# Optimization experiments

Hardware: AMD Instinct MI355X
Metric: run time of the kernel (lower is better)

Reference implementation:

```python
import jax, jax.numpy as jnp
import numpy as np

BETA = 0.9
THRESHOLD = 1.0


def setup_inputs() -> dict:
    key = jax.random.key(0)
    k1, k2 = jax.random.split(key)
    T, N_IN, N_OUT = 1024, 4096, 4096
    x = jax.random.normal(k1, (T, N_IN), dtype=jnp.float32)
    # fc1 weight initialized uniform[0,1), shape [out, in] like nn.Linear
    W = jax.random.uniform(k2, (N_OUT, N_IN), dtype=jnp.float32)
    return {"x": x, "W": W}


def reference(x, W):
    # Precompute the batched linear projection over all timesteps: [T, N_OUT]
    cur = jnp.einsum('ti,oi->to', x, W)
    mem0 = jnp.zeros((W.shape[0],), dtype=x.dtype)

    def step(mem, c):
        # snntorch Leaky, reset_mechanism='subtract':
        # reset is computed from the PREVIOUS membrane potential (detached)
        reset = (mem > THRESHOLD).astype(mem.dtype)
        mem_new = BETA * mem + c - reset * THRESHOLD
        spk = (mem_new > THRESHOLD).astype(mem.dtype)
        return mem_new, (spk, mem_new)

    _, (spk_rec, mem_rec) = jax.lax.scan(step, mem0, cur)
    return spk_rec, mem_rec
```

## Files before the change

kernel.cpp:

```cpp
#include <hip/hip_runtime.h>
#include <hip/hip_bf16.h>
#include <stdint.h>


typedef __attribute__((ext_vector_type(8))) short bf16x8;
typedef __attribute__((ext_vector_type(4))) float floatx4;

#define T_STEPS 1024
#define N_IN    4096
#define N_OUT   4096

#define PH_T 128
#define NPH  (T_STEPS / PH_T)
#define NB_N 16
#define TP   132

#define TN ((size_t)T_STEPS * N_OUT)

__device__ __forceinline__ unsigned short f2bf_rne(float f) {
    unsigned int u = __builtin_bit_cast(unsigned int, f);
    unsigned int r = 0x7FFFu + ((u >> 16) & 1u);
    return (unsigned short)((u + r) >> 16);
}

__global__ __launch_bounds__(256) void cvt2_kernel(const float4* __restrict__ inX,
                                                   ushort4* __restrict__ outX, int n4x,
                                                   const float4* __restrict__ inW,
                                                   ushort4* __restrict__ outW, int n4w) {
    int i = blockIdx.x * blockDim.x + threadIdx.x;
    const float4* in;
    ushort4* out;
    int k;
    if (i < n4x) { in = inX; out = outX; k = i; }
    else         { in = inW; out = outW; k = i - n4x; if (k >= n4w) return; }
    float4 v = in[k];
    ushort4 o;
    o.x = f2bf_rne(v.x);
    o.y = f2bf_rne(v.y);
    o.z = f2bf_rne(v.z);
    o.w = f2bf_rne(v.w);
    out[k] = o;
}

__device__ __forceinline__ void gload16(const void* g, void* l) {
    __builtin_amdgcn_global_load_lds((const __attribute__((address_space(1))) void*)g,
                                     (__attribute__((address_space(3))) void*)l,
                                     16, 0, 0);
}

#define SB0()  __builtin_amdgcn_sched_barrier(0)
#define BARR() __builtin_amdgcn_s_barrier()

__global__ __launch_bounds__(512, 2) void gemm8(const short* __restrict__ A,
                                                const short* __restrict__ B,
                                                unsigned short* __restrict__ Pb,
                                                int kLen) {
    __shared__ short lds[65536];

    const int tid  = threadIdx.x;
    const int lane = tid & 63;
    const int wv   = tid >> 6;
    const int wm   = (wv >> 2) * 128;
    const int wn   = (wv & 3) * 64;

    const int bid  = blockIdx.x;
    const int z    = bid >> 6;
    const int tile = bid & 63;
    const long bm  = (long)(tile >> 4) * 256;
    const long bn  = (long)(tile & 15) * 256;
    const int kBeg = z * kLen;
    unsigned short* __restrict__ Pz = Pb + (size_t)z * TN;
    const int NT    = kLen / 64;
    const int NITER = NT / 2;

    const int srow = lane >> 3;
    const int scol = ((lane & 7) ^ srow) << 3;
    const short* aSrc = A + (bm + wv * 8 + srow) * (long)N_IN + kBeg + scol;
    const short* bSrc = B + (bn + wv * 8 + srow) * (long)N_IN + kBeg + scol;
    const int ldA = wv * 512;
    const int ldB = 32768 + wv * 512;

    const int fm    = lane & 15;
    const int fko   = (lane >> 4) * 8;
    const int cbase = fko ^ ((fm & 7) << 3);

    floatx4 acc[8][4] = {};
    bf16x8 af[4][2];
    bf16x8 bq[2][2][2];

    auto loadA = [&](int b, int qm) {
#pragma unroll
        for (int mi = 0; mi < 4; ++mi)
#pragma unroll
            for (int ks = 0; ks < 2; ++ks)
                af[mi][ks] = *(const bf16x8*)(
                    lds + b * 16384 + (wm + qm * 64 + mi * 16 + fm) * 64 +
                    (cbase ^ (ks << 5)));
    };
    auto loadB = [&](int b, int qn) {
#pragma unroll
        for (int nj = 0; nj < 2; ++nj)
#pragma unroll
            for (int ks = 0; ks < 2; ++ks)
                bq[qn][nj][ks] = *(const bf16x8*)(
                    lds + 32768 + b * 16384 + (wn + qn * 32 + nj * 16 + fm) * 64 +
                    (cbase ^ (ks << 5)));
    };
    auto mfma16 = [&](int qm, int qn) {
        __builtin_amdgcn_s_setprio(1);
#pragma unroll
        for (int ks = 0; ks < 2; ++ks)
#pragma unroll
            for (int mi = 0; mi < 4; ++mi)
#pragma unroll
                for (int nj = 0; nj < 2; ++nj)
                    acc[qm * 4 + mi][qn * 2 + nj] =
                        __builtin_amdgcn_mfma_f32_16x16x32_bf16(
                            af[mi][ks], bq[qn][nj][ks],
                            acc[qm * 4 + mi][qn * 2 + nj], 0, 0, 0);
        __builtin_amdgcn_s_setprio(0);
    };
    auto stageA = [&](int b, int h, int t) {
        const short* s = aSrc + (size_t)(h * 128) * N_IN + t * 64;
        gload16(s,                    lds + b * 16384 + h * 8192 + ldA);
        gload16(s + (size_t)64 * N_IN, lds + b * 16384 + h * 8192 + 4096 + ldA);
    };
    auto stageB = [&](int b, int h, int t) {
        const short* s = bSrc + (size_t)(h * 128) * N_IN + t * 64;
        gload16(s,                    lds + b * 16384 + h * 8192 + ldB);
        gload16(s + (size_t)64 * N_IN, lds + b * 16384 + h * 8192 + 4096 + ldB);
    };
    const int cn = lane & 15;
    const int cm = (lane >> 4) * 4;
    auto storeQuad = [&](int qm, int qn) {
#pragma unroll
        for (int mi = 0; mi < 4; ++mi)
#pragma unroll
            for (int nj = 0; nj < 2; ++nj) {
                const floatx4 a = acc[qm * 4 + mi][qn * 2 + nj];
                unsigned int lo = (unsigned int)f2bf_rne(a[0]) |
                                  ((unsigned int)f2bf_rne(a[1]) << 16);
                unsigned int hi = (unsigned int)f2bf_rne(a[2]) |
                                  ((unsigned int)f2bf_rne(a[3]) << 16);
                uint2 v; v.x = lo; v.y = hi;
                size_t nIdx = (size_t)(bn + wn + qn * 32 + nj * 16 + cn);
                *(uint2*)(Pz + nIdx * T_STEPS +
                          (size_t)(bm + wm + qm * 64 + mi * 16 + cm)) = v;
            }
    };

    stageA(0, 0, 0); stageA(0, 1, 0);
    stageB(0, 0, 0); stageB(0, 1, 0);
    stageB(1, 0, 1); stageB(1, 1, 1);
    asm volatile("s_waitcnt vmcnt(4)" ::: "memory");
    SB0();
    BARR();

    for (int i = 0; i < NITER - 1; ++i) {
        const int t1 = 2 * i + 1;
        const int t2 = 2 * i + 2;
        const int t3 = 2 * i + 3;

        loadA(0, 0); loadB(0, 0);
        stageA(1, 0, t1);
        asm volatile("s_waitcnt lgkmcnt(8)" ::: "memory");
        SB0(); BARR();
        asm volatile("s_waitcnt lgkmcnt(0)" ::: "memory"); SB0();
        mfma16(0, 0);
        SB0(); BARR();

        loadB(0, 1);
        stageA(1, 1, t1);
        SB0(); BARR();
        asm volatile("s_waitcnt lgkmcnt(0)" ::: "memory"); SB0();
        mfma16(0, 1);
        SB0(); BARR();

        loadA(0, 1);
        stageB(0, 0, t2);
        SB0(); BARR();
        asm volatile("s_waitcnt lgkmcnt(0)" ::: "memory"); SB0();
        mfma16(1, 0);
        SB0(); BARR();

        stageB(0, 1, t2);
        SB0(); BARR();
        mfma16(1, 1);
        asm volatile("s_waitcnt vmcnt(4)" ::: "memory");
        SB0(); BARR();

        loadA(1, 0); loadB(1, 0);
        stageA(0, 0, t2);
        asm volatile("s_waitcnt lgkmcnt(8)" ::: "memory");
        SB0(); BARR();
        asm volatile("s_waitcnt lgkmcnt(0)" ::: "memory"); SB0();
        mfma16(0, 0);
        SB0(); BARR();

        loadB(1, 1);
        stageA(0, 1, t2);
        SB0(); BARR();
        asm volatile("s_waitcnt lgkmcnt(0)" ::: "memory"); SB0();
        mfma16(0, 1);
        SB0(); BARR();

        loadA(1, 1);
        stageB(1, 0, t3);
        SB0(); BARR();
        asm volatile("s_waitcnt lgkmcnt(0)" ::: "memory"); SB0();
        mfma16(1, 0);
        SB0(); BARR();

        stageB(1, 1, t3);
        SB0(); BARR();
        mfma16(1, 1);
        asm volatile("s_waitcnt vmcnt(4)" ::: "memory");
        SB0(); BARR();
    }

    {
        const int t1 = 2 * (NITER - 1) + 1;

        loadA(0, 0); loadB(0, 0);
        stageA(1, 0, t1);
        asm volatile("s_waitcnt lgkmcnt(8)" ::: "memory");
        SB0(); BARR();
        asm volatile("s_waitcnt lgkmcnt(0)" ::: "memory"); SB0();
        mfma16(0, 0);
        SB0(); BARR();

        loadB(0, 1);
        stageA(1, 1, t1);
        SB0(); BARR();
        asm volatile("s_waitcnt lgkmcnt(0)" ::: "memory"); SB0();
        mfma16(0, 1);
        SB0(); BARR();

        loadA(0, 1);
        SB0(); BARR();
        asm volatile("s_waitcnt lgkmcnt(0)" ::: "memory"); SB0();
        mfma16(1, 0);
        SB0(); BARR();

        SB0(); BARR();
        mfma16(1, 1);
        asm volatile("s_waitcnt vmcnt(0)" ::: "memory");
        SB0(); BARR();

        loadA(1, 0); loadB(1, 0);
        asm volatile("s_waitcnt lgkmcnt(8)" ::: "memory");
        SB0(); BARR();
        asm volatile("s_waitcnt lgkmcnt(0)" ::: "memory"); SB0();
        mfma16(0, 0);
        storeQuad(0, 0);
        SB0(); BARR();

        loadB(1, 1);
        SB0(); BARR();
        asm volatile("s_waitcnt lgkmcnt(0)" ::: "memory"); SB0();
        mfma16(0, 1);
        storeQuad(0, 1);
        SB0(); BARR();

        loadA(1, 1);
        SB0(); BARR();
        asm volatile("s_waitcnt lgkmcnt(0)" ::: "memory"); SB0();
        mfma16(1, 0);
        storeQuad(1, 0);
        SB0(); BARR();

        SB0(); BARR();
        mfma16(1, 1);
        storeQuad(1, 1);
    }
}

template <int NPART>
__global__ __launch_bounds__(512) void scan_kernel(const unsigned short* __restrict__ Pb,
                                                   float* __restrict__ out) {
    __shared__ float ringCur[2][NB_N * TP];
    __shared__ float ringMem[2][NB_N * TP];

    const int tid  = threadIdx.x;
    const int wv   = tid >> 6;
    const int lane = tid & 63;
    const int n0   = blockIdx.x * NB_N;

    const int pn = lane & 15;

    const int sn = tid >> 4;
    const int sc = tid & 15;

    float mem = 0.0f;

    auto stage = [&](int buf, size_t tb) {
        float s[8];
#pragma unroll
        for (int j = 0; j < 8; ++j) s[j] = 0.0f;
#pragma unroll
        for (int zz = 0; zz < NPART; ++zz) {
            const uint4 v = *(const uint4*)(Pb + (size_t)zz * TN +
                                            (size_t)(n0 + sn) * T_STEPS + tb + sc * 8);
            unsigned int w0 = v.x, w1 = v.y, w2 = v.z, w3 = v.w;
            s[0] += __builtin_bit_cast(float, w0 << 16);
            s[1] += __builtin_bit_cast(float, w0 & 0xFFFF0000u);
            s[2] += __builtin_bit_cast(float, w1 << 16);
            s[3] += __builtin_bit_cast(float, w1 & 0xFFFF0000u);
            s[4] += __builtin_bit_cast(float, w2 << 16);
            s[5] += __builtin_bit_cast(float, w2 & 0xFFFF0000u);
            s[6] += __builtin_bit_cast(float, w3 << 16);
            s[7] += __builtin_bit_cast(float, w3 & 0xFFFF0000u);
        }
        float4 f0; f0.x = s[0]; f0.y = s[1]; f0.z = s[2]; f0.w = s[3];
        float4 f1; f1.x = s[4]; f1.y = s[5]; f1.z = s[6]; f1.w = s[7];
        float* rc = &ringCur[buf][sn * TP + sc * 8];
        *(float4*)rc = f0;
        *(float4*)(rc + 4) = f1;
    };

    auto writeOut = [&](int buf, size_t tb) {
        const float* mr = ringMem[buf];
        for (int it = tid; it < 512; it += 448) {
            int t  = it >> 2;
            int nq = it & 3;
            float m0 = mr[(nq * 4 + 0) * TP + t];
            float m1 = mr[(nq * 4 + 1) * TP + t];
            float m2 = mr[(nq * 4 + 2) * TP + t];
            float m3 = mr[(nq * 4 + 3) * TP + t];
            float4 mv; mv.x = m0; mv.y = m1; mv.z = m2; mv.w = m3;
            float4 sv;
            sv.x = m0 > 1.0f ? 1.0f : 0.0f;
            sv.y = m1 > 1.0f ? 1.0f : 0.0f;
            sv.z = m2 > 1.0f ? 1.0f : 0.0f;
            sv.w = m3 > 1.0f ? 1.0f : 0.0f;
            size_t idx = (tb + t) * N_OUT + n0 + nq * 4;
            *(float4*)&out[idx]      = sv;
            *(float4*)&out[TN + idx] = mv;
        }
    };

    if (tid < 256) stage(0, 0);
    __syncthreads();

    for (int ph = 0; ph < NPH; ++ph) {
        if (wv < 7) {
            if (ph >= 1) writeOut((ph - 1) & 1, (size_t)(ph - 1) * PH_T);
            if (tid < 256 && ph + 1 < NPH)
                stage((ph + 1) & 1, (size_t)(ph + 1) * PH_T);
        } else if (lane < 16) {
            const float* base = &ringCur[ph & 1][pn * TP];
            float* mbase = &ringMem[ph & 1][pn * TP];
#pragma unroll
            for (int sub = 0; sub < 4; ++sub) {
                float2 buf[16];
#pragma unroll
                for (int q = 0; q < 16; ++q)
                    buf[q] = *(const float2*)&base[sub * 32 + q * 2];
#pragma unroll
                for (int q = 0; q < 16; ++q) {
                    float rst = mem > 1.0f ? 1.0f : 0.0f;
                    mem = fmaf(0.9f, mem, buf[q].x) - rst;
                    float m0 = mem;
                    rst = mem > 1.0f ? 1.0f : 0.0f;
                    mem = fmaf(0.9f, mem, buf[q].y) - rst;
                    float2 mo; mo.x = m0; mo.y = mem;
                    *(float2*)&mbase[sub * 32 + q * 2] = mo;
                }
            }
        }
        __syncthreads();
    }

    if (wv < 7) writeOut((NPH - 1) & 1, (size_t)(NPH - 1) * PH_T);
}

extern "C" void kernel_launch(void* const* d_in, const int* in_sizes, int n_in,
                              void* d_out, int out_size, void* d_ws, size_t ws_size,
                              hipStream_t stream) {
    const float* x = (const float*)d_in[0];
    const float* W = (const float*)d_in[1];
    float* out = (float*)d_out;

    char* ws = (char*)d_ws;
    const size_t xbBytes = (size_t)T_STEPS * N_IN * 2;
    const size_t WbBytes = (size_t)N_OUT * N_IN * 2;
    const size_t PBytes  = TN * 2;
    short* xb = (short*)ws;
    short* Wb = (short*)(ws + xbBytes);
    unsigned short* Pb = (unsigned short*)(ws + xbBytes + WbBytes);

    int S = 1;
    if (ws_size >= xbBytes + WbBytes + 4 * PBytes)      S = 4;
    else if (ws_size >= xbBytes + WbBytes + 2 * PBytes) S = 2;

    {
        const int n4x = T_STEPS * N_IN / 4;
        const int n4w = N_OUT * N_IN / 4;
        const int nthr = n4x + n4w;
        cvt2_kernel<<<(nthr + 255) / 256, 256, 0, stream>>>(
            (const float4*)x, (ushort4*)xb, n4x,
            (const float4*)W, (ushort4*)Wb, n4w);
    }

    gemm8<<<64 * S, 512, 0, stream>>>(xb, Wb, Pb, N_IN / S);

    if (S == 4)      scan_kernel<4><<<N_OUT / NB_N, 512, 0, stream>>>(Pb, out);
    else if (S == 2) scan_kernel<2><<<N_OUT / NB_N, 512, 0, stream>>>(Pb, out);
    else             scan_kernel<1><<<N_OUT / NB_N, 512, 0, stream>>>(Pb, out);
}
```

Before: 168.8 us.

## Fuse W fp32-to-bf16 conversion into GEMM B-tile staging via registers

Drops the separate conversion pass over W. The GEMM now loads fp32 W tiles into registers, converts them to bf16 and writes them swizzled into LDS, interleaved with the existing pipeline. This avoids a full fp32 read plus bf16 write and re-read of the 4096x4096 weight matrix in the conversion kernel. In exchange the GEMM reads twice as many bytes for B, moving B through registers instead of direct global-to-LDS loads. It also adds more register pressure and extra vmcnt waits inside the main loop.

```diff
diff --git a/kernel.cpp b/kernel.cpp
--- a/kernel.cpp
+++ b/kernel.cpp
@@ -23,23 +23,17 @@
     return (unsigned short)((u + r) >> 16);
 }
 
-__global__ __launch_bounds__(256) void cvt2_kernel(const float4* __restrict__ inX,
-                                                   ushort4* __restrict__ outX, int n4x,
-                                                   const float4* __restrict__ inW,
-                                                   ushort4* __restrict__ outW, int n4w) {
+__global__ __launch_bounds__(256) void cvt_x(const float4* __restrict__ in,
+                                             ushort4* __restrict__ out, int n4) {
     int i = blockIdx.x * blockDim.x + threadIdx.x;
-    const float4* in;
-    ushort4* out;
-    int k;
-    if (i < n4x) { in = inX; out = outX; k = i; }
-    else         { in = inW; out = outW; k = i - n4x; if (k >= n4w) return; }
-    float4 v = in[k];
+    if (i >= n4) return;
+    float4 v = in[i];
     ushort4 o;
     o.x = f2bf_rne(v.x);
     o.y = f2bf_rne(v.y);
     o.z = f2bf_rne(v.z);
     o.w = f2bf_rne(v.w);
-    out[k] = o;
+    out[i] = o;
 }
 
 __device__ __forceinline__ void gload16(const void* g, void* l) {
@@ -52,7 +46,7 @@
 #define BARR() __builtin_amdgcn_s_barrier()
 
 __global__ __launch_bounds__(512, 2) void gemm8(const short* __restrict__ A,
-                                                const short* __restrict__ B,
+                                                const float* __restrict__ Wf,
                                                 unsigned short* __restrict__ Pb,
                                                 int kLen) {
     __shared__ short lds[65536];
@@ -76,9 +70,12 @@
     const int srow = lane >> 3;
     const int scol = ((lane & 7) ^ srow) << 3;
     const short* aSrc = A + (bm + wv * 8 + srow) * (long)N_IN + kBeg + scol;
-    const short* bSrc = B + (bn + wv * 8 + srow) * (long)N_IN + kBeg + scol;
     const int ldA = wv * 512;
-    const int ldB = 32768 + wv * 512;
+
+    const int brow = tid >> 2;
+    const int bcq  = tid & 3;
+    const float* wBase = Wf + (size_t)(bn + brow) * N_IN + kBeg + bcq * 16;
+    const int bsw = brow & 7;
 
     const int fm    = lane & 15;
     const int fko   = (lane >> 4) * 8;
@@ -87,6 +84,7 @@
     floatx4 acc[8][4] = {};
     bf16x8 af[4][2];
     bf16x8 bq[2][2][2];
+    float4 b0h0[4], b0h1[4], b1h0[4], b1h1[4];
 
     auto loadA = [&](int b, int qm) {
 #pragma unroll
@@ -122,13 +120,28 @@
     };
     auto stageA = [&](int b, int h, int t) {
         const short* s = aSrc + (size_t)(h * 128) * N_IN + t * 64;
-        gload16(s,                    lds + b * 16384 + h * 8192 + ldA);
+        gload16(s,                     lds + b * 16384 + h * 8192 + ldA);
         gload16(s + (size_t)64 * N_IN, lds + b * 16384 + h * 8192 + 4096 + ldA);
     };
-    auto stageB = [&](int b, int h, int t) {
-        const short* s = bSrc + (size_t)(h * 128) * N_IN + t * 64;
-        gload16(s,                    lds + b * 16384 + h * 8192 + ldB);
-        gload16(s + (size_t)64 * N_IN, lds + b * 16384 + h * 8192 + 4096 + ldB);
+    auto gldB = [&](int h, int t, float4* r) {
+        const float* s = wBase + (size_t)(h * 128) * N_IN + t * 64;
+#pragma unroll
+        for (int j = 0; j < 4; ++j) r[j] = *(const float4*)(s + j * 4);
+    };
+    auto cwrB = [&](int b, int h, const float4* r) {
+        unsigned int w[8];
+#pragma unroll
+        for (int j = 0; j < 4; ++j) {
+            w[2 * j]     = (unsigned int)f2bf_rne(r[j].x) |
+                           ((unsigned int)f2bf_rne(r[j].y) << 16);
+            w[2 * j + 1] = (unsigned int)f2bf_rne(r[j].z) |
+                           ((unsigned int)f2bf_rne(r[j].w) << 16);
+        }
+        short* base = lds + 32768 + b * 16384 + h * 8192 + brow * 64;
+        uint4 v0; v0.x = w[0]; v0.y = w[1]; v0.z = w[2]; v0.w = w[3];
+        uint4 v1; v1.x = w[4]; v1.y = w[5]; v1.z = w[6]; v1.w = w[7];
+        *(uint4*)(base + (((bcq * 2)     ^ bsw) * 8)) = v0;
+        *(uint4*)(base + (((bcq * 2 + 1) ^ bsw) * 8)) = v1;
     };
     const int cn = lane & 15;
     const int cm = (lane >> 4) * 4;
@@ -150,10 +163,15 @@
     };
 
     stageA(0, 0, 0); stageA(0, 1, 0);
-    stageB(0, 0, 0); stageB(0, 1, 0);
-    stageB(1, 0, 1); stageB(1, 1, 1);
-    asm volatile("s_waitcnt vmcnt(4)" ::: "memory");
-    SB0();
+    gldB(0, 0, b0h0); gldB(1, 0, b0h1);
+    gldB(0, 1, b1h0); gldB(1, 1, b1h1);
+    asm volatile("s_waitcnt vmcnt(12)" ::: "memory"); SB0();
+    cwrB(0, 0, b0h0);
+    asm volatile("s_waitcnt vmcnt(8)" ::: "memory"); SB0();
+    cwrB(0, 1, b0h1);
+    asm volatile("s_waitcnt vmcnt(4)" ::: "memory"); SB0();
+    cwrB(1, 0, b1h0);
+    asm volatile("s_waitcnt lgkmcnt(0)" ::: "memory"); SB0();
     BARR();
 
     for (int i = 0; i < NITER - 1; ++i) {
@@ -162,6 +180,8 @@
         const int t3 = 2 * i + 3;
 
         loadA(0, 0); loadB(0, 0);
+        asm volatile("s_waitcnt vmcnt(0)" ::: "memory"); SB0();
+        cwrB(1, 1, b1h1);
         stageA(1, 0, t1);
         asm volatile("s_waitcnt lgkmcnt(8)" ::: "memory");
         SB0(); BARR();
@@ -177,19 +197,23 @@
         SB0(); BARR();
 
         loadA(0, 1);
-        stageB(0, 0, t2);
+        gldB(0, t2, b0h0);
         SB0(); BARR();
         asm volatile("s_waitcnt lgkmcnt(0)" ::: "memory"); SB0();
         mfma16(1, 0);
         SB0(); BARR();
 
-        stageB(0, 1, t2);
+        gldB(1, t2, b0h1);
         SB0(); BARR();
         mfma16(1, 1);
-        asm volatile("s_waitcnt vmcnt(4)" ::: "memory");
+        asm volatile("s_waitcnt vmcnt(4)" ::: "memory"); SB0();
+        cwrB(0, 0, b0h0);
+        asm volatile("s_waitcnt lgkmcnt(0)" ::: "memory");
         SB0(); BARR();
 
         loadA(1, 0); loadB(1, 0);
+        asm volatile("s_waitcnt vmcnt(0)" ::: "memory"); SB0();
+        cwrB(0, 1, b0h1);
         stageA(0, 0, t2);
         asm volatile("s_waitcnt lgkmcnt(8)" ::: "memory");
         SB0(); BARR();
@@ -205,16 +229,18 @@
         SB0(); BARR();
 
         loadA(1, 1);
-        stageB(1, 0, t3);
+        gldB(0, t3, b1h0);
         SB0(); BARR();
         asm volatile("s_waitcnt lgkmcnt(0)" ::: "memory"); SB0();
         mfma16(1, 0);
         SB0(); BARR();
 
-        stageB(1, 1, t3);
+        gldB(1, t3, b1h1);
         SB0(); BARR();
         mfma16(1, 1);
-        asm volatile("s_waitcnt vmcnt(4)" ::: "memory");
+        asm volatile("s_waitcnt vmcnt(4)" ::: "memory"); SB0();
+        cwrB(1, 0, b1h0);
+        asm volatile("s_waitcnt lgkmcnt(0)" ::: "memory");
         SB0(); BARR();
     }
 
@@ -222,6 +248,8 @@
         const int t1 = 2 * (NITER - 1) + 1;
 
         loadA(0, 0); loadB(0, 0);
+        asm volatile("s_waitcnt vmcnt(0)" ::: "memory"); SB0();
+        cwrB(1, 1, b1h1);
         stageA(1, 0, t1);
         asm volatile("s_waitcnt lgkmcnt(8)" ::: "memory");
         SB0(); BARR();
@@ -383,26 +411,21 @@
 
     char* ws = (char*)d_ws;
     const size_t xbBytes = (size_t)T_STEPS * N_IN * 2;
-    const size_t WbBytes = (size_t)N_OUT * N_IN * 2;
     const size_t PBytes  = TN * 2;
     short* xb = (short*)ws;
-    short* Wb = (short*)(ws + xbBytes);
-    unsigned short* Pb = (unsigned short*)(ws + xbBytes + WbBytes);
+    unsigned short* Pb = (unsigned short*)(ws + xbBytes);
 
     int S = 1;
-    if (ws_size >= xbBytes + WbBytes + 4 * PBytes)      S = 4;
-    else if (ws_size >= xbBytes + WbBytes + 2 * PBytes) S = 2;
+    if (ws_size >= xbBytes + 4 * PBytes)      S = 4;
+    else if (ws_size >= xbBytes + 2 * PBytes) S = 2;
 
     {
         const int n4x = T_STEPS * N_IN / 4;
-        const int n4w = N_OUT * N_IN / 4;
-        const int nthr = n4x + n4w;
-        cvt2_kernel<<<(nthr + 255) / 256, 256, 0, stream>>>(
-            (const float4*)x, (ushort4*)xb, n4x,
-            (const float4*)W, (ushort4*)Wb, n4w);
+        cvt_x<<<(n4x + 255) / 256, 256, 0, stream>>>(
+            (const float4*)x, (ushort4*)xb, n4x);
     }
 
-    gemm8<<<64 * S, 512, 0, stream>>>(xb, Wb, Pb, N_IN / S);
+    gemm8<<<64 * S, 512, 0, stream>>>(xb, W, Pb, N_IN / S);
 
     if (S == 4)      scan_kernel<4><<<N_OUT / NB_N, 512, 0, stream>>>(Pb, out);
     else if (S == 2) scan_kernel<2><<<N_OUT / NB_N, 512, 0, stream>>>(Pb, out);
```

Result: slower. 187.5 us (+11.1%).
